# Kernel tuning notes

Measured on AMD Instinct MI355X. Metric: run time of the kernel, lower is better.

The kernel has to match this reference:

```python
import jax, jax.numpy as jnp
import numpy as np

IN_DIM = 64
B, C, H, W = 4, IN_DIM, 64, 64
KEY_CH = IN_DIM // 8  # softmax scale channel count (as in torch code)


def conv1x1(x, w, b):
    # x: [B,C,H,W], w: [O,C], b: [O] -> [B,O,H,W]
    return jnp.einsum('bchw,oc->bohw', x, w) + b[None, :, None, None]


def setup_inputs() -> dict:
    key = jax.random.key(0)
    ks = jax.random.split(key, 24)
    s = 0.05
    d16, d4 = IN_DIM // 16, IN_DIM // 4
    inp = {
        'input1': jax.random.normal(ks[0], (B, C, H, W), jnp.float32),
        'input2': jax.random.normal(ks[1], (B, C, H, W), jnp.float32),
        'wq1': jax.random.normal(ks[2], (d16, C), jnp.float32) * s,
        'bq1': jax.random.normal(ks[3], (d16,), jnp.float32) * s,
        'wq2': jax.random.normal(ks[4], (d16, C), jnp.float32) * s,
        'bq2': jax.random.normal(ks[5], (d16,), jnp.float32) * s,
        'wq3': jax.random.normal(ks[6], (d16, C), jnp.float32) * s,
        'bq3': jax.random.normal(ks[7], (d16,), jnp.float32) * s,
        'wq4': jax.random.normal(ks[8], (d16, C), jnp.float32) * s,
        'bq4': jax.random.normal(ks[9], (d16,), jnp.float32) * s,
        'wk': jax.random.normal(ks[10], (d4, C), jnp.float32) * s,
        'bk': jax.random.normal(ks[11], (d4,), jnp.float32) * s,
        'wv': jax.random.normal(ks[12], (C, C), jnp.float32) * s,
        'bv': jax.random.normal(ks[13], (C,), jnp.float32) * s,
        'wk2': jax.random.normal(ks[14], (d4, C), jnp.float32) * s,
        'bk2': jax.random.normal(ks[15], (d4,), jnp.float32) * s,
        'wv2': jax.random.normal(ks[16], (C, C), jnp.float32) * s,
        'bv2': jax.random.normal(ks[17], (C,), jnp.float32) * s,
        'gamma': jax.random.normal(ks[18], (1,), jnp.float32) * 0.1,
    }
    return inp


def _branch(q_in, feat, wk_, bk_, wv_, bv_, gamma, resid):
    b, c, h, w = feat.shape
    n = h * w
    scale = KEY_CH ** (-0.5)
    q = q_in.reshape(b, -1, n).transpose(0, 2, 1)            # [B,N,C/4]
    k = conv1x1(feat, wk_, bk_).reshape(b, -1, n)            # [B,C/4,N]
    attn = jax.nn.softmax(scale * jnp.einsum('bnd,bdm->bnm', q, k), axis=-1)  # [B,N,N]
    v = conv1x1(feat, wv_, bv_).reshape(b, c, n)             # [B,C,N]
    out = jnp.einsum('bcn,bmn->bcm', v, attn).reshape(b, c, h, w)
    return gamma[0] * out + resid


def reference(input1, input2, wq1, bq1, wq2, bq2, wq3, bq3, wq4, bq4,
              wk, bk, wv, bv, wk2, bk2, wv2, bv2, gamma):
    input3 = input1 + (input2 - input1) / 3
    input4 = input3 + (input2 - input1) / 3
    q1 = conv1x1(input1, wq1, bq1)
    q2 = conv1x1(input2, wq2, bq2)
    q3 = conv1x1(input3, wq3, bq3)
    q4 = conv1x1(input4, wq4, bq4)
    q_in1 = jnp.concatenate([q1, q3, q4, q2], axis=1)  # [B,C/4,H,W]
    q_in2 = jnp.concatenate([q2, q4, q3, q1], axis=1)
    out1 = _branch(q_in1, input1, wk, bk, wv, bv, gamma, input1)
    out2 = _branch(q_in2, input2, wk2, bk2, wv2, bv2, gamma, input2)
    return out1, out2
```

## Files before the change

### kernel.cpp

```cpp
#include <hip/hip_runtime.h>
#include <hip/hip_bf16.h>
#include <stdint.h>

typedef short bf16x8 __attribute__((ext_vector_type(8)));
typedef float f32x4  __attribute__((ext_vector_type(4)));
typedef float f32x16 __attribute__((ext_vector_type(16)));
typedef unsigned int u32;

#define N_SP 4096
#define QSCALE 0.5100697284f

__device__ inline unsigned short f2bf(float f) {
    unsigned u = __float_as_uint(f);
    u += 0x7fff + ((u >> 16) & 1);
    return (unsigned short)(u >> 16);
}
__device__ inline float bf2f(short s) {
    return __uint_as_float(((unsigned)(unsigned short)s) << 16);
}
__device__ inline u32 cvtpk_bf16(float lo, float hi) {
    u32 r;
    asm("v_cvt_pk_bf16_f32 %0, %1, %2" : "=v"(r) : "v"(lo), "v"(hi));
    return r;
}
__device__ inline void pl32swap(u32& a, u32& b) {
    asm volatile("v_permlane32_swap_b32 %0, %1" : "+v"(a), "+v"(b));
}


__global__ __launch_bounds__(256) void stage1_kernel(
    const float* __restrict__ in1, const float* __restrict__ in2,
    const float* __restrict__ wq1, const float* __restrict__ bq1,
    const float* __restrict__ wq2, const float* __restrict__ bq2,
    const float* __restrict__ wq3, const float* __restrict__ bq3,
    const float* __restrict__ wq4, const float* __restrict__ bq4,
    const float* __restrict__ wk,  const float* __restrict__ bk,
    const float* __restrict__ wv,  const float* __restrict__ bv,
    const float* __restrict__ wk2, const float* __restrict__ bk2,
    const float* __restrict__ wv2, const float* __restrict__ bv2,
    unsigned short* __restrict__ Qs, unsigned short* __restrict__ Ks,
    unsigned short* __restrict__ Vs)
{
    __shared__ unsigned short w1h[16][64];
    __shared__ unsigned short w2h[16][64];
    __shared__ unsigned short wkh[16][64];
    __shared__ unsigned short wvh[64][64];
    __shared__ float qb[16], kbb[16], vbb[64];

    const int bid = blockIdx.x;
    const int br = bid & 7;
    const int ntl = bid >> 3;
    const int b = br >> 1, rr = br & 1;
    const int tid = threadIdx.x;

    const float* wqs[4]; const float* bqs[4]; float c1s[4], c2s[4];
    if (rr == 0) {
        wqs[0]=wq1; bqs[0]=bq1; c1s[0]=1.f;       c2s[0]=0.f;
        wqs[1]=wq3; bqs[1]=bq3; c1s[1]=2.f/3.f;   c2s[1]=1.f/3.f;
        wqs[2]=wq4; bqs[2]=bq4; c1s[2]=1.f/3.f;   c2s[2]=2.f/3.f;
        wqs[3]=wq2; bqs[3]=bq2; c1s[3]=0.f;       c2s[3]=1.f;
    } else {
        wqs[0]=wq2; bqs[0]=bq2; c1s[0]=0.f;       c2s[0]=1.f;
        wqs[1]=wq4; bqs[1]=bq4; c1s[1]=1.f/3.f;   c2s[1]=2.f/3.f;
        wqs[2]=wq3; bqs[2]=bq3; c1s[2]=2.f/3.f;   c2s[2]=1.f/3.f;
        wqs[3]=wq1; bqs[3]=bq1; c1s[3]=1.f;       c2s[3]=0.f;
    }
    const float* wkp = rr ? wk2 : wk;  const float* bkp = rr ? bk2 : bk;
    const float* wvp = rr ? wv2 : wv;  const float* bvp = rr ? bv2 : bv;

    for (int e = tid; e < 1024; e += 256) {
        int g = e >> 8;
        int h = e >> 6;
        int ch = e & 63;
        float wq_ = wqs[g][e & 255];
        w1h[h][ch] = f2bf(c1s[g] * wq_ * QSCALE);
        w2h[h][ch] = f2bf(c2s[g] * wq_ * QSCALE);
        wkh[h][ch] = f2bf(wkp[e]);
    }
    for (int e = tid; e < 4096; e += 256) wvh[e >> 6][e & 63] = f2bf(wvp[e]);
    if (tid < 16) { qb[tid] = bqs[tid >> 2][tid & 3] * QSCALE; kbb[tid] = bkp[tid]; }
    if (tid < 64) vbb[tid] = bvp[tid];
    __syncthreads();

    const int nl = tid & 31;
    const int og = tid >> 5;
    const int n = ntl * 32 + nl;
    const float* x1p = in1 + (size_t)b * 64 * N_SP + n;
    const float* x2p = in2 + (size_t)b * 64 * N_SP + n;
    const float* xfp = rr ? x2p : x1p;

    if (og < 2) {
        float acc[8];
        #pragma unroll
        for (int o = 0; o < 8; o++) acc[o] = qb[og * 8 + o];
        for (int g = 0; g < 8; g++) {
            float x1v[8], x2v[8];
            #pragma unroll
            for (int cc = 0; cc < 8; cc++) {
                x1v[cc] = x1p[(size_t)(g * 8 + cc) * N_SP];
                x2v[cc] = x2p[(size_t)(g * 8 + cc) * N_SP];
            }
            #pragma unroll
            for (int o = 0; o < 8; o++) {
                bf16x8 w1v = *(const bf16x8*)(&w1h[og * 8 + o][g * 8]);
                bf16x8 w2v = *(const bf16x8*)(&w2h[og * 8 + o][g * 8]);
                #pragma unroll
                for (int cc = 0; cc < 8; cc++)
                    acc[o] += bf2f(w1v[cc]) * x1v[cc] + bf2f(w2v[cc]) * x2v[cc];
            }
        }
        bf16x8 qv;
        #pragma unroll
        for (int o = 0; o < 8; o++) qv[o] = (short)f2bf(acc[o]);
        *(bf16x8*)(Qs + (size_t)br * 65536 + ntl * 512 + og * 256 + nl * 8) = qv;
    } else if (og < 4) {
        const int dg = og - 2;
        float acc[8];
        #pragma unroll
        for (int o = 0; o < 8; o++) acc[o] = kbb[dg * 8 + o];
        for (int g = 0; g < 8; g++) {
            float xfv[8];
            #pragma unroll
            for (int cc = 0; cc < 8; cc++) xfv[cc] = xfp[(size_t)(g * 8 + cc) * N_SP];
            #pragma unroll
            for (int o = 0; o < 8; o++) {
                bf16x8 wkv = *(const bf16x8*)(&wkh[dg * 8 + o][g * 8]);
                #pragma unroll
                for (int cc = 0; cc < 8; cc++)
                    acc[o] += bf2f(wkv[cc]) * xfv[cc];
            }
        }
        bf16x8 kv;
        #pragma unroll
        for (int o = 0; o < 8; o++) kv[o] = (short)f2bf(acc[o]);
        *(bf16x8*)(Ks + (size_t)br * 65536 + ntl * 512 + nl * 16 + dg * 8) = kv;
    } else {
        const int cg = og - 4;
        float acc[16];
        #pragma unroll
        for (int j = 0; j < 16; j++) acc[j] = vbb[cg * 16 + j];
        for (int g = 0; g < 8; g++) {
            float xfv[8];
            #pragma unroll
            for (int cc = 0; cc < 8; cc++) xfv[cc] = xfp[(size_t)(g * 8 + cc) * N_SP];
            #pragma unroll
            for (int j = 0; j < 16; j++) {
                bf16x8 wvv = *(const bf16x8*)(&wvh[cg * 16 + j][g * 8]);
                #pragma unroll
                for (int cc = 0; cc < 8; cc++)
                    acc[j] += bf2f(wvv[cc]) * xfv[cc];
            }
        }
        size_t basen = (size_t)br * 262144 + (size_t)(n >> 5) * 2048 +
                       (size_t)((n >> 4) & 1) * 1024 + (size_t)((n >> 3) & 1) * 256 +
                       (n & 7);
        #pragma unroll
        for (int j = 0; j < 16; j++) {
            int c = cg * 16 + j;
            Vs[basen + (c >> 5) * 512 + (c & 31) * 8] = f2bf(acc[j]);
        }
    }
}

__global__ __launch_bounds__(256, 4) void attn_kernel(
    const unsigned short* __restrict__ Qs, const unsigned short* __restrict__ Ks,
    const unsigned short* __restrict__ Vs,
    const float* __restrict__ in1, const float* __restrict__ in2,
    const float* __restrict__ gamma_p, float* __restrict__ out)
{
    __shared__ float accb[4][64][33];
    __shared__ float rsl[4][32];
    __shared__ float invl[32];

    const int bid = blockIdx.x;
    const int br = bid & 7;
    const int qt = bid >> 3;
    const int b = br >> 1, rr = br & 1;
    const int tid = threadIdx.x;
    const int ks = tid >> 6;
    const int l = tid & 63;
    const int q31 = l & 31, hi = l >> 5;

    const unsigned short* Qb = Qs + (size_t)br * 65536;
    const unsigned short* Kb = Ks + (size_t)br * 65536;
    const unsigned short* Vb = Vs + (size_t)br * 262144;

    const bf16x8 aq = *(const bf16x8*)(Qb + qt * 512 + l * 8);

    f32x16 accA = {0,0,0,0,0,0,0,0,0,0,0,0,0,0,0,0};
    f32x16 accB = {0,0,0,0,0,0,0,0,0,0,0,0,0,0,0,0};
    float rsum = 0.f;

    const int koff = q31 * 16 + hi * 8;

    bf16x8 kf[2];
    bf16x8 vf[2][4];
    {
        const unsigned short* kp = Kb + (size_t)(ks * 32) * 512;
        const unsigned short* vp = Vb + (size_t)(ks * 32) * 2048;
        kf[0] = *(const bf16x8*)(kp + koff);
        #pragma unroll
        for (int j = 0; j < 4; j++) vf[0][j] = *(const bf16x8*)(vp + j * 512 + l * 8);
    }

    #pragma unroll
    for (int t = 0; t < 32; ++t) {
        const int cur = t & 1, nxt = cur ^ 1;
        const int tn = (t < 31) ? t + 1 : 31;
        {
            const unsigned short* kpn = Kb + (size_t)(ks * 32 + tn) * 512;
            const unsigned short* vpn = Vb + (size_t)(ks * 32 + tn) * 2048;
            kf[nxt] = *(const bf16x8*)(kpn + koff);
            #pragma unroll
            for (int j = 0; j < 4; j++) vf[nxt][j] = *(const bf16x8*)(vpn + j * 512 + l * 8);
        }

        const f32x16 z16 = {0,0,0,0,0,0,0,0,0,0,0,0,0,0,0,0};
        f32x16 s = __builtin_amdgcn_mfma_f32_32x32x16_bf16(kf[cur], aq, z16, 0, 0, 0);

        float p[16];
        #pragma unroll
        for (int r2 = 0; r2 < 16; ++r2) {
            p[r2] = exp2f(s[r2]);
            rsum += p[r2];
        }

        u32 a0 = cvtpk_bf16(p[0], p[1]);   u32 a2 = cvtpk_bf16(p[4], p[5]);
        pl32swap(a0, a2);
        u32 a1 = cvtpk_bf16(p[2], p[3]);   u32 a3 = cvtpk_bf16(p[6], p[7]);
        pl32swap(a1, a3);
        u32 c0 = cvtpk_bf16(p[8], p[9]);   u32 c2 = cvtpk_bf16(p[12], p[13]);
        pl32swap(c0, c2);
        u32 c1 = cvtpk_bf16(p[10], p[11]); u32 c3 = cvtpk_bf16(p[14], p[15]);
        pl32swap(c1, c3);

        union U { u32 w[4]; bf16x8 v; };
        U u0; u0.w[0] = a0; u0.w[1] = a1; u0.w[2] = a2; u0.w[3] = a3;
        U u1; u1.w[0] = c0; u1.w[1] = c1; u1.w[2] = c2; u1.w[3] = c3;

        accA = __builtin_amdgcn_mfma_f32_32x32x16_bf16(u0.v, vf[cur][0], accA, 0, 0, 0);
        accB = __builtin_amdgcn_mfma_f32_32x32x16_bf16(u0.v, vf[cur][1], accB, 0, 0, 0);
        accA = __builtin_amdgcn_mfma_f32_32x32x16_bf16(u1.v, vf[cur][2], accA, 0, 0, 0);
        accB = __builtin_amdgcn_mfma_f32_32x32x16_bf16(u1.v, vf[cur][3], accB, 0, 0, 0);
    }

    rsum += __shfl_xor(rsum, 32, 64);
    if (l < 32) rsl[ks][l] = rsum;

    #pragma unroll
    for (int r2 = 0; r2 < 16; ++r2) {
        int qrow = (r2 & 3) + 8 * (r2 >> 2) + 4 * hi;
        accb[ks][q31][qrow]      = accA[r2];
        accb[ks][32 + q31][qrow] = accB[r2];
    }
    __syncthreads();

    if (tid < 32)
        invl[tid] = 1.0f / (rsl[0][tid] + rsl[1][tid] + rsl[2][tid] + rsl[3][tid]);
    __syncthreads();

    const float g = gamma_p[0];
    const int c = tid >> 2, mg = tid & 3;
    const float* fp = (rr ? in2 : in1) + (size_t)b * 64 * N_SP + (size_t)c * N_SP +
                      qt * 32 + mg * 8;
    float* op = out + (size_t)rr * (4ull * 64 * N_SP) + (size_t)b * 64 * N_SP +
                (size_t)c * N_SP + qt * 32 + mg * 8;

    float ov[8];
    #pragma unroll
    for (int i = 0; i < 8; i++) {
        int q = mg * 8 + i;
        ov[i] = (accb[0][c][q] + accb[1][c][q] + accb[2][c][q] + accb[3][c][q]) * invl[q];
    }
    f32x4 f0 = *(const f32x4*)fp;
    f32x4 f1 = *(const f32x4*)(fp + 4);
    f32x4 o0, o1;
    #pragma unroll
    for (int i = 0; i < 4; i++) {
        o0[i] = g * ov[i]     + f0[i];
        o1[i] = g * ov[4 + i] + f1[i];
    }
    *(f32x4*)op = o0;
    *(f32x4*)(op + 4) = o1;
}

extern "C" void kernel_launch(void* const* d_in, const int* in_sizes, int n_in,
                              void* d_out, int out_size, void* d_ws, size_t ws_size,
                              hipStream_t stream) {
    const float* in1 = (const float*)d_in[0];
    const float* in2 = (const float*)d_in[1];
    const float* wq1 = (const float*)d_in[2];  const float* bq1 = (const float*)d_in[3];
    const float* wq2 = (const float*)d_in[4];  const float* bq2 = (const float*)d_in[5];
    const float* wq3 = (const float*)d_in[6];  const float* bq3 = (const float*)d_in[7];
    const float* wq4 = (const float*)d_in[8];  const float* bq4 = (const float*)d_in[9];
    const float* wk  = (const float*)d_in[10]; const float* bk  = (const float*)d_in[11];
    const float* wv  = (const float*)d_in[12]; const float* bv  = (const float*)d_in[13];
    const float* wk2 = (const float*)d_in[14]; const float* bk2 = (const float*)d_in[15];
    const float* wv2 = (const float*)d_in[16]; const float* bv2 = (const float*)d_in[17];
    const float* gamma_p = (const float*)d_in[18];

    unsigned short* Qs = (unsigned short*)d_ws;
    unsigned short* Ks = Qs + (size_t)8 * 65536;
    unsigned short* Vs = Ks + (size_t)8 * 65536;

    stage1_kernel<<<dim3(1024), 256, 0, stream>>>(in1, in2, wq1, bq1, wq2, bq2,
                                                  wq3, bq3, wq4, bq4, wk, bk, wv, bv,
                                                  wk2, bk2, wv2, bv2, Qs, Ks, Vs);
    attn_kernel<<<dim3(1024), 256, 0, stream>>>(Qs, Ks, Vs, in1, in2, gamma_p,
                                                (float*)d_out);
}
```

Measured before the change: 150.7 us.

## Reuse K/V tiles across four query tiles per block and restructure projection kernel

The attention kernel now handles four 32-query tiles per block with 8 waves, each wave covering 16 key tiles, so each K/V fragment load is reused across four QK and PV MFMA chains. This cuts global K/V traffic and grid size, at the cost of more accumulator registers and four serialized epilogues with barriers. The projection kernel drops the shared-memory bf16 weight staging in favour of fp32 weights read directly from global memory, uses 512-thread blocks over 64 spatial positions, and changes the K store layout. Softmax uses the raw exp2 builtin with tree-summed row sums.

```diff
diff --git a/kernel.cpp b/kernel.cpp
--- a/kernel.cpp
+++ b/kernel.cpp
@@ -15,9 +15,6 @@
     u += 0x7fff + ((u >> 16) & 1);
     return (unsigned short)(u >> 16);
 }
-__device__ inline float bf2f(short s) {
-    return __uint_as_float(((unsigned)(unsigned short)s) << 16);
-}
 __device__ inline u32 cvtpk_bf16(float lo, float hi) {
     u32 r;
     asm("v_cvt_pk_bf16_f32 %0, %1, %2" : "=v"(r) : "v"(lo), "v"(hi));
@@ -27,8 +24,10 @@
     asm volatile("v_permlane32_swap_b32 %0, %1" : "+v"(a), "+v"(b));
 }
 
-
-__global__ __launch_bounds__(256) void stage1_kernel(
+union U { u32 w[4]; bf16x8 v; };
+
+
+__global__ __launch_bounds__(512, 4) void stage1_kernel(
     const float* __restrict__ in1, const float* __restrict__ in2,
     const float* __restrict__ wq1, const float* __restrict__ bq1,
     const float* __restrict__ wq2, const float* __restrict__ bq2,
@@ -41,17 +40,19 @@
     unsigned short* __restrict__ Qs, unsigned short* __restrict__ Ks,
     unsigned short* __restrict__ Vs)
 {
-    __shared__ unsigned short w1h[16][64];
-    __shared__ unsigned short w2h[16][64];
-    __shared__ unsigned short wkh[16][64];
-    __shared__ unsigned short wvh[64][64];
-    __shared__ float qb[16], kbb[16], vbb[64];
-
     const int bid = blockIdx.x;
     const int br = bid & 7;
     const int ntl = bid >> 3;
     const int b = br >> 1, rr = br & 1;
     const int tid = threadIdx.x;
+    const int og = tid >> 6;
+    const int nl = tid & 63;
+    const int n = ntl * 64 + nl;
+    const int nt = n >> 5, nl32 = n & 31;
+
+    const float* x1p = in1 + (size_t)b * 64 * N_SP + n;
+    const float* x2p = in2 + (size_t)b * 64 * N_SP + n;
+    const float* xfp = rr ? x2p : x1p;
 
     const float* wqs[4]; const float* bqs[4]; float c1s[4], c2s[4];
     if (rr == 0) {
@@ -68,116 +69,160 @@
     const float* wkp = rr ? wk2 : wk;  const float* bkp = rr ? bk2 : bk;
     const float* wvp = rr ? wv2 : wv;  const float* bvp = rr ? bv2 : bv;
 
-    for (int e = tid; e < 1024; e += 256) {
-        int g = e >> 8;
-        int h = e >> 6;
-        int ch = e & 63;
-        float wq_ = wqs[g][e & 255];
-        w1h[h][ch] = f2bf(c1s[g] * wq_ * QSCALE);
-        w2h[h][ch] = f2bf(c2s[g] * wq_ * QSCALE);
-        wkh[h][ch] = f2bf(wkp[e]);
-    }
-    for (int e = tid; e < 4096; e += 256) wvh[e >> 6][e & 63] = f2bf(wvp[e]);
-    if (tid < 16) { qb[tid] = bqs[tid >> 2][tid & 3] * QSCALE; kbb[tid] = bkp[tid]; }
-    if (tid < 64) vbb[tid] = bvp[tid];
-    __syncthreads();
-
-    const int nl = tid & 31;
-    const int og = tid >> 5;
-    const int n = ntl * 32 + nl;
-    const float* x1p = in1 + (size_t)b * 64 * N_SP + n;
-    const float* x2p = in2 + (size_t)b * 64 * N_SP + n;
-    const float* xfp = rr ? x2p : x1p;
-
     if (og < 2) {
+        const int gA = og * 2, gB = og * 2 + 1;
+        const float* wA = wqs[gA]; const float* wB = wqs[gB];
+        const float c1A = c1s[gA], c2A = c2s[gA];
+        const float c1B = c1s[gB], c2B = c2s[gB];
         float acc[8];
         #pragma unroll
-        for (int o = 0; o < 8; o++) acc[o] = qb[og * 8 + o];
-        for (int g = 0; g < 8; g++) {
-            float x1v[8], x2v[8];
-            #pragma unroll
-            for (int cc = 0; cc < 8; cc++) {
-                x1v[cc] = x1p[(size_t)(g * 8 + cc) * N_SP];
-                x2v[cc] = x2p[(size_t)(g * 8 + cc) * N_SP];
+        for (int o = 0; o < 8; o++) acc[o] = 0.f;
+        #pragma unroll
+        for (int half = 0; half < 2; half++) {
+            float xa[32], xb[32];
+            #pragma unroll
+            for (int cc = 0; cc < 32; cc++) {
+                float x1 = x1p[(size_t)(half * 32 + cc) * N_SP];
+                float x2 = x2p[(size_t)(half * 32 + cc) * N_SP];
+                xa[cc] = c1A * x1 + c2A * x2;
+                xb[cc] = c1B * x1 + c2B * x2;
             }
             #pragma unroll
-            for (int o = 0; o < 8; o++) {
-                bf16x8 w1v = *(const bf16x8*)(&w1h[og * 8 + o][g * 8]);
-                bf16x8 w2v = *(const bf16x8*)(&w2h[og * 8 + o][g * 8]);
+            for (int o = 0; o < 4; o++) {
                 #pragma unroll
-                for (int cc = 0; cc < 8; cc++)
-                    acc[o] += bf2f(w1v[cc]) * x1v[cc] + bf2f(w2v[cc]) * x2v[cc];
+                for (int cc = 0; cc < 32; cc++) {
+                    acc[o]     += wA[o * 64 + half * 32 + cc] * xa[cc];
+                    acc[4 + o] += wB[o * 64 + half * 32 + cc] * xb[cc];
+                }
             }
         }
         bf16x8 qv;
         #pragma unroll
-        for (int o = 0; o < 8; o++) qv[o] = (short)f2bf(acc[o]);
-        *(bf16x8*)(Qs + (size_t)br * 65536 + ntl * 512 + og * 256 + nl * 8) = qv;
+        for (int o = 0; o < 8; o++) {
+            float bias = (o < 4) ? bqs[gA][o] : bqs[gB][o - 4];
+            qv[o] = (short)f2bf((acc[o] + bias) * QSCALE);
+        }
+        *(bf16x8*)(Qs + (size_t)br * 65536 + nt * 512 + og * 256 + nl32 * 8) = qv;
     } else if (og < 4) {
         const int dg = og - 2;
         float acc[8];
         #pragma unroll
-        for (int o = 0; o < 8; o++) acc[o] = kbb[dg * 8 + o];
-        for (int g = 0; g < 8; g++) {
-            float xfv[8];
-            #pragma unroll
-            for (int cc = 0; cc < 8; cc++) xfv[cc] = xfp[(size_t)(g * 8 + cc) * N_SP];
+        for (int o = 0; o < 8; o++) acc[o] = 0.f;
+        #pragma unroll
+        for (int half = 0; half < 2; half++) {
+            float xf[32];
+            #pragma unroll
+            for (int cc = 0; cc < 32; cc++) xf[cc] = xfp[(size_t)(half * 32 + cc) * N_SP];
             #pragma unroll
             for (int o = 0; o < 8; o++) {
-                bf16x8 wkv = *(const bf16x8*)(&wkh[dg * 8 + o][g * 8]);
                 #pragma unroll
-                for (int cc = 0; cc < 8; cc++)
-                    acc[o] += bf2f(wkv[cc]) * xfv[cc];
+                for (int cc = 0; cc < 32; cc++)
+                    acc[o] += wkp[(dg * 8 + o) * 64 + half * 32 + cc] * xf[cc];
             }
         }
         bf16x8 kv;
         #pragma unroll
-        for (int o = 0; o < 8; o++) kv[o] = (short)f2bf(acc[o]);
-        *(bf16x8*)(Ks + (size_t)br * 65536 + ntl * 512 + nl * 16 + dg * 8) = kv;
+        for (int o = 0; o < 8; o++) kv[o] = (short)f2bf(acc[o] + bkp[dg * 8 + o]);
+        *(bf16x8*)(Ks + (size_t)br * 65536 + nt * 512 + dg * 256 + nl32 * 8) = kv;
     } else {
         const int cg = og - 4;
         float acc[16];
         #pragma unroll
-        for (int j = 0; j < 16; j++) acc[j] = vbb[cg * 16 + j];
-        for (int g = 0; g < 8; g++) {
-            float xfv[8];
-            #pragma unroll
-            for (int cc = 0; cc < 8; cc++) xfv[cc] = xfp[(size_t)(g * 8 + cc) * N_SP];
-            #pragma unroll
-            for (int j = 0; j < 16; j++) {
-                bf16x8 wvv = *(const bf16x8*)(&wvh[cg * 16 + j][g * 8]);
+        for (int o = 0; o < 16; o++) acc[o] = 0.f;
+        #pragma unroll
+        for (int half = 0; half < 2; half++) {
+            float xf[32];
+            #pragma unroll
+            for (int cc = 0; cc < 32; cc++) xf[cc] = xfp[(size_t)(half * 32 + cc) * N_SP];
+            #pragma unroll
+            for (int o = 0; o < 16; o++) {
                 #pragma unroll
-                for (int cc = 0; cc < 8; cc++)
-                    acc[j] += bf2f(wvv[cc]) * xfv[cc];
+                for (int cc = 0; cc < 32; cc++)
+                    acc[o] += wvp[(cg * 16 + o) * 64 + half * 32 + cc] * xf[cc];
             }
         }
-        size_t basen = (size_t)br * 262144 + (size_t)(n >> 5) * 2048 +
-                       (size_t)((n >> 4) & 1) * 1024 + (size_t)((n >> 3) & 1) * 256 +
-                       (n & 7);
-        #pragma unroll
-        for (int j = 0; j < 16; j++) {
-            int c = cg * 16 + j;
-            Vs[basen + (c >> 5) * 512 + (c & 31) * 8] = f2bf(acc[j]);
+        const int kt = (n >> 4) & 1;
+        size_t vb = (size_t)br * 262144 + (size_t)nt * 2048 +
+                    (size_t)((n >> 3) & 1) * 256 + (n & 7);
+        #pragma unroll
+        for (int o = 0; o < 16; o++) {
+            int c = cg * 16 + o;
+            Vs[vb + (size_t)((kt * 2 + (c >> 5)) * 512 + (c & 31) * 8)] =
+                f2bf(acc[o] + bvp[c]);
         }
     }
 }
 
-__global__ __launch_bounds__(256, 4) void attn_kernel(
+#define SOFTPV(QT, ACCA, ACCB) do {                                               \
+    f32x16 s_ = __builtin_amdgcn_mfma_f32_32x32x16_bf16(kfA, aq##QT, z16, 0, 0, 0); \
+    float p_[16];                                                                 \
+    _Pragma("unroll")                                                             \
+    for (int r_ = 0; r_ < 16; ++r_) p_[r_] = __builtin_amdgcn_exp2f(s_[r_]);      \
+    rsum##QT += (((p_[0]+p_[1])+(p_[2]+p_[3]))+((p_[4]+p_[5])+(p_[6]+p_[7])))     \
+              + (((p_[8]+p_[9])+(p_[10]+p_[11]))+((p_[12]+p_[13])+(p_[14]+p_[15]))); \
+    u32 a0 = cvtpk_bf16(p_[0], p_[1]),  a2 = cvtpk_bf16(p_[4], p_[5]);            \
+    pl32swap(a0, a2);                                                             \
+    u32 a1 = cvtpk_bf16(p_[2], p_[3]),  a3 = cvtpk_bf16(p_[6], p_[7]);            \
+    pl32swap(a1, a3);                                                             \
+    u32 c0 = cvtpk_bf16(p_[8], p_[9]),  c2 = cvtpk_bf16(p_[12], p_[13]);          \
+    pl32swap(c0, c2);                                                             \
+    u32 c1 = cvtpk_bf16(p_[10], p_[11]), c3 = cvtpk_bf16(p_[14], p_[15]);         \
+    pl32swap(c1, c3);                                                             \
+    U u0_, u1_;                                                                   \
+    u0_.w[0]=a0; u0_.w[1]=a1; u0_.w[2]=a2; u0_.w[3]=a3;                           \
+    u1_.w[0]=c0; u1_.w[1]=c1; u1_.w[2]=c2; u1_.w[3]=c3;                           \
+    ACCA = __builtin_amdgcn_mfma_f32_32x32x16_bf16(u0_.v, vf0, ACCA, 0, 0, 0);    \
+    ACCB = __builtin_amdgcn_mfma_f32_32x32x16_bf16(u0_.v, vf1, ACCB, 0, 0, 0);    \
+    ACCA = __builtin_amdgcn_mfma_f32_32x32x16_bf16(u1_.v, vf2, ACCA, 0, 0, 0);    \
+    ACCB = __builtin_amdgcn_mfma_f32_32x32x16_bf16(u1_.v, vf3, ACCB, 0, 0, 0);    \
+} while (0)
+
+#define EPI(QT, ACCA, ACCB) do {                                                  \
+    float rs_ = rsum##QT + __shfl_xor(rsum##QT, 32, 64);                          \
+    if (l < 32) rsl[w][l] = rs_;                                                  \
+    _Pragma("unroll")                                                             \
+    for (int r_ = 0; r_ < 16; ++r_) {                                             \
+        int qrow_ = (r_ & 3) + 8 * (r_ >> 2) + 4 * hi;                            \
+        accb[w][q31][qrow_]      = ACCA[r_];                                      \
+        accb[w][32 + q31][qrow_] = ACCB[r_];                                      \
+    }                                                                             \
+    __syncthreads();                                                              \
+    if (tid < 32) invl[tid] = 1.0f /                                              \
+        (((rsl[0][tid]+rsl[1][tid])+(rsl[2][tid]+rsl[3][tid])) +                  \
+         ((rsl[4][tid]+rsl[5][tid])+(rsl[6][tid]+rsl[7][tid])));                  \
+    __syncthreads();                                                              \
+    {                                                                             \
+        const int c_ = tid >> 3, mg_ = tid & 7;                                   \
+        const int m_ = qq * 128 + (QT) * 32 + mg_ * 4;                            \
+        f32x4 o_;                                                                 \
+        _Pragma("unroll")                                                         \
+        for (int mi_ = 0; mi_ < 4; ++mi_) {                                       \
+            int q_ = mg_ * 4 + mi_;                                               \
+            float v_ = ((accb[0][c_][q_]+accb[1][c_][q_])+(accb[2][c_][q_]+accb[3][c_][q_])) \
+                     + ((accb[4][c_][q_]+accb[5][c_][q_])+(accb[6][c_][q_]+accb[7][c_][q_])); \
+            o_[mi_] = g * (v_ * invl[q_]) + featp[(size_t)c_ * N_SP + m_ + mi_];  \
+        }                                                                         \
+        *(f32x4*)(outp + (size_t)c_ * N_SP + m_) = o_;                            \
+    }                                                                             \
+    __syncthreads();                                                              \
+} while (0)
+
+__global__ __launch_bounds__(512, 2) void attn_kernel(
     const unsigned short* __restrict__ Qs, const unsigned short* __restrict__ Ks,
     const unsigned short* __restrict__ Vs,
     const float* __restrict__ in1, const float* __restrict__ in2,
     const float* __restrict__ gamma_p, float* __restrict__ out)
 {
-    __shared__ float accb[4][64][33];
-    __shared__ float rsl[4][32];
+    __shared__ float accb[8][64][33];
+    __shared__ float rsl[8][32];
     __shared__ float invl[32];
 
     const int bid = blockIdx.x;
     const int br = bid & 7;
-    const int qt = bid >> 3;
+    const int qq = bid >> 3;
     const int b = br >> 1, rr = br & 1;
     const int tid = threadIdx.x;
-    const int ks = tid >> 6;
+    const int w = tid >> 6;
     const int l = tid & 63;
     const int q31 = l & 31, hi = l >> 5;
 
@@ -185,103 +230,48 @@
     const unsigned short* Kb = Ks + (size_t)br * 65536;
     const unsigned short* Vb = Vs + (size_t)br * 262144;
 
-    const bf16x8 aq = *(const bf16x8*)(Qb + qt * 512 + l * 8);
-
-    f32x16 accA = {0,0,0,0,0,0,0,0,0,0,0,0,0,0,0,0};
-    f32x16 accB = {0,0,0,0,0,0,0,0,0,0,0,0,0,0,0,0};
-    float rsum = 0.f;
-
-    const int koff = q31 * 16 + hi * 8;
-
-    bf16x8 kf[2];
-    bf16x8 vf[2][4];
-    {
-        const unsigned short* kp = Kb + (size_t)(ks * 32) * 512;
-        const unsigned short* vp = Vb + (size_t)(ks * 32) * 2048;
-        kf[0] = *(const bf16x8*)(kp + koff);
-        #pragma unroll
-        for (int j = 0; j < 4; j++) vf[0][j] = *(const bf16x8*)(vp + j * 512 + l * 8);
+    const bf16x8 aq0 = *(const bf16x8*)(Qb + (size_t)(qq * 4 + 0) * 512 + l * 8);
+    const bf16x8 aq1 = *(const bf16x8*)(Qb + (size_t)(qq * 4 + 1) * 512 + l * 8);
+    const bf16x8 aq2 = *(const bf16x8*)(Qb + (size_t)(qq * 4 + 2) * 512 + l * 8);
+    const bf16x8 aq3 = *(const bf16x8*)(Qb + (size_t)(qq * 4 + 3) * 512 + l * 8);
+
+    const f32x16 z16 = {0,0,0,0,0,0,0,0,0,0,0,0,0,0,0,0};
+    f32x16 acc00 = z16, acc01 = z16;
+    f32x16 acc10 = z16, acc11 = z16;
+    f32x16 acc20 = z16, acc21 = z16;
+    f32x16 acc30 = z16, acc31 = z16;
+    float rsum0 = 0.f, rsum1 = 0.f, rsum2 = 0.f, rsum3 = 0.f;
+
+    const unsigned short* kbase = Kb + (size_t)(w * 16) * 512 + l * 8;
+    const unsigned short* vbase = Vb + (size_t)(w * 16) * 2048 + l * 8;
+
+    bf16x8 kfA = *(const bf16x8*)kbase;
+    #pragma unroll 1
+    for (int t = 0; t < 16; ++t) {
+        bf16x8 vf0 = *(const bf16x8*)(vbase);
+        bf16x8 vf1 = *(const bf16x8*)(vbase + 512);
+        bf16x8 vf2 = *(const bf16x8*)(vbase + 1024);
+        bf16x8 vf3 = *(const bf16x8*)(vbase + 1536);
+        bf16x8 kfN = *(const bf16x8*)(kbase + 512);
+
+        SOFTPV(0, acc00, acc01);
+        SOFTPV(1, acc10, acc11);
+        SOFTPV(2, acc20, acc21);
+        SOFTPV(3, acc30, acc31);
+
+        kfA = kfN;
+        kbase += 512;
+        vbase += 2048;
     }
 
-    #pragma unroll
-    for (int t = 0; t < 32; ++t) {
-        const int cur = t & 1, nxt = cur ^ 1;
-        const int tn = (t < 31) ? t + 1 : 31;
-        {
-            const unsigned short* kpn = Kb + (size_t)(ks * 32 + tn) * 512;
-            const unsigned short* vpn = Vb + (size_t)(ks * 32 + tn) * 2048;
-            kf[nxt] = *(const bf16x8*)(kpn + koff);
-            #pragma unroll
-            for (int j = 0; j < 4; j++) vf[nxt][j] = *(const bf16x8*)(vpn + j * 512 + l * 8);
-        }
-
-        const f32x16 z16 = {0,0,0,0,0,0,0,0,0,0,0,0,0,0,0,0};
-        f32x16 s = __builtin_amdgcn_mfma_f32_32x32x16_bf16(kf[cur], aq, z16, 0, 0, 0);
-
-        float p[16];
-        #pragma unroll
-        for (int r2 = 0; r2 < 16; ++r2) {
-            p[r2] = exp2f(s[r2]);
-            rsum += p[r2];
-        }
-
-        u32 a0 = cvtpk_bf16(p[0], p[1]);   u32 a2 = cvtpk_bf16(p[4], p[5]);
-        pl32swap(a0, a2);
-        u32 a1 = cvtpk_bf16(p[2], p[3]);   u32 a3 = cvtpk_bf16(p[6], p[7]);
-        pl32swap(a1, a3);
-        u32 c0 = cvtpk_bf16(p[8], p[9]);   u32 c2 = cvtpk_bf16(p[12], p[13]);
-        pl32swap(c0, c2);
-        u32 c1 = cvtpk_bf16(p[10], p[11]); u32 c3 = cvtpk_bf16(p[14], p[15]);
-        pl32swap(c1, c3);
-
-        union U { u32 w[4]; bf16x8 v; };
-        U u0; u0.w[0] = a0; u0.w[1] = a1; u0.w[2] = a2; u0.w[3] = a3;
-        U u1; u1.w[0] = c0; u1.w[1] = c1; u1.w[2] = c2; u1.w[3] = c3;
-
-        accA = __builtin_amdgcn_mfma_f32_32x32x16_bf16(u0.v, vf[cur][0], accA, 0, 0, 0);
-        accB = __builtin_amdgcn_mfma_f32_32x32x16_bf16(u0.v, vf[cur][1], accB, 0, 0, 0);
-        accA = __builtin_amdgcn_mfma_f32_32x32x16_bf16(u1.v, vf[cur][2], accA, 0, 0, 0);
-        accB = __builtin_amdgcn_mfma_f32_32x32x16_bf16(u1.v, vf[cur][3], accB, 0, 0, 0);
-    }
-
-    rsum += __shfl_xor(rsum, 32, 64);
-    if (l < 32) rsl[ks][l] = rsum;
-
-    #pragma unroll
-    for (int r2 = 0; r2 < 16; ++r2) {
-        int qrow = (r2 & 3) + 8 * (r2 >> 2) + 4 * hi;
-        accb[ks][q31][qrow]      = accA[r2];
-        accb[ks][32 + q31][qrow] = accB[r2];
-    }
-    __syncthreads();
-
-    if (tid < 32)
-        invl[tid] = 1.0f / (rsl[0][tid] + rsl[1][tid] + rsl[2][tid] + rsl[3][tid]);
-    __syncthreads();
-
     const float g = gamma_p[0];
-    const int c = tid >> 2, mg = tid & 3;
-    const float* fp = (rr ? in2 : in1) + (size_t)b * 64 * N_SP + (size_t)c * N_SP +
-                      qt * 32 + mg * 8;
-    float* op = out + (size_t)rr * (4ull * 64 * N_SP) + (size_t)b * 64 * N_SP +
-                (size_t)c * N_SP + qt * 32 + mg * 8;
-
-    float ov[8];
-    #pragma unroll
-    for (int i = 0; i < 8; i++) {
-        int q = mg * 8 + i;
-        ov[i] = (accb[0][c][q] + accb[1][c][q] + accb[2][c][q] + accb[3][c][q]) * invl[q];
-    }
-    f32x4 f0 = *(const f32x4*)fp;
-    f32x4 f1 = *(const f32x4*)(fp + 4);
-    f32x4 o0, o1;
-    #pragma unroll
-    for (int i = 0; i < 4; i++) {
-        o0[i] = g * ov[i]     + f0[i];
-        o1[i] = g * ov[4 + i] + f1[i];
-    }
-    *(f32x4*)op = o0;
-    *(f32x4*)(op + 4) = o1;
+    const float* featp = (rr ? in2 : in1) + (size_t)b * 64 * N_SP;
+    float* outp = out + (size_t)rr * (4ull * 64 * N_SP) + (size_t)b * 64 * N_SP;
+
+    EPI(0, acc00, acc01);
+    EPI(1, acc10, acc11);
+    EPI(2, acc20, acc21);
+    EPI(3, acc30, acc31);
 }
 
 extern "C" void kernel_launch(void* const* d_in, const int* in_sizes, int n_in,
@@ -303,9 +293,9 @@
     unsigned short* Ks = Qs + (size_t)8 * 65536;
     unsigned short* Vs = Ks + (size_t)8 * 65536;
 
-    stage1_kernel<<<dim3(1024), 256, 0, stream>>>(in1, in2, wq1, bq1, wq2, bq2,
-                                                  wq3, bq3, wq4, bq4, wk, bk, wv, bv,
-                                                  wk2, bk2, wv2, bv2, Qs, Ks, Vs);
-    attn_kernel<<<dim3(1024), 256, 0, stream>>>(Qs, Ks, Vs, in1, in2, gamma_p,
-                                                (float*)d_out);
-}
+    stage1_kernel<<<dim3(512), 512, 0, stream>>>(in1, in2, wq1, bq1, wq2, bq2,
+                                                 wq3, bq3, wq4, bq4, wk, bk, wv, bv,
+                                                 wk2, bk2, wv2, bv2, Qs, Ks, Vs);
+    attn_kernel<<<dim3(256), 512, 0, stream>>>(Qs, Ks, Vs, in1, in2, gamma_p,
+                                               (float*)d_out);
+}
```

Measured after the change: 176.7 us. 1.17x slower.
